# Kernel tuning notes

Measured on AMD Instinct MI355X. Metric: run time of the kernel, lower is better.

## Reference

```python
import jax, jax.numpy as jnp
import numpy as np

B, S, H = 32, 2048, 1024


def setup_inputs() -> dict:
    key = jax.random.key(0)
    ks = jax.random.split(key, 7)
    return {
        "query": jax.random.normal(ks[0], (B, 1, H), dtype=jnp.float32),
        "key": jax.random.normal(ks[1], (S, B, H), dtype=jnp.float32),
        "Wa_w": jax.random.normal(ks[2], (H, H), dtype=jnp.float32) / np.sqrt(H),
        "Wa_b": jax.random.normal(ks[3], (H,), dtype=jnp.float32) * 0.01,
        "Ua_w": jax.random.normal(ks[4], (H, H), dtype=jnp.float32) / np.sqrt(H),
        "Ua_b": jax.random.normal(ks[5], (H,), dtype=jnp.float32) * 0.01,
        "va_w": jax.random.normal(ks[6], (H,), dtype=jnp.float32) / np.sqrt(H),
        "va_b": jnp.zeros((1,), dtype=jnp.float32),
    }


def reference(query, key, Wa_w, Wa_b, Ua_w, Ua_b, va_w, va_b):
    # key: (S, B, H) -> (B, S, H)
    k = jnp.transpose(key, (1, 0, 2))
    # additive (Bahdanau) energies: tanh(Wa q + Ua k), broadcast over S
    e = jnp.tanh((query @ Wa_w + Wa_b) + (k @ Ua_w + Ua_b))  # (B, S, H)
    scores = jnp.einsum("bsh,h->bs", e, va_w) + va_b[0]       # (B, S)
    weights = jax.nn.softmax(scores, axis=-1)[:, None, :]      # (B, 1, S)
    context = jnp.einsum("bqs,bsh->bqh", weights, k)           # (B, 1, H)
    return context, weights
```

## Files before the change

### kernel.cpp

```cpp
#include <hip/hip_runtime.h>

#define Hdim 1024
#define Bdim 32
#define Sdim 2048

typedef __attribute__((ext_vector_type(8))) __bf16 bf16x8;
typedef __attribute__((ext_vector_type(4))) __bf16 bf16x4;
typedef __attribute__((ext_vector_type(4))) float f32x4;

#define GLOAD_LDS16(gp, lp)                                                              \
  __builtin_amdgcn_global_load_lds(                                                     \
      (const __attribute__((address_space(1))) unsigned int*)(gp),                      \
      (__attribute__((address_space(3))) unsigned int*)(lp), 16, 0, 0)

__global__ __launch_bounds__(256) void convert_key_kernel(const float* __restrict__ key,
                                                          __bf16* __restrict__ bkey) {
  size_t base = (size_t)blockIdx.x * 512 + threadIdx.x;
  const float4* src = (const float4*)key;
  float4 f0 = src[base];
  float4 f1 = src[base + 256];
  bf16x4 a, b;
  a[0] = (__bf16)f0.x; a[1] = (__bf16)f0.y; a[2] = (__bf16)f0.z; a[3] = (__bf16)f0.w;
  b[0] = (__bf16)f1.x; b[1] = (__bf16)f1.y; b[2] = (__bf16)f1.z; b[3] = (__bf16)f1.w;
  bf16x4* dst = (bf16x4*)bkey;
  dst[base] = a;
  dst[base + 256] = b;
}

__global__ __launch_bounds__(256) void convert_ua_kernel(const float* __restrict__ Ua,
                                                         __bf16* __restrict__ ubt) {
  int du = blockIdx.x * 256 + threadIdx.x;
  int n  = du & 127;
  int k8 = (du >> 7) & 127;
  int nt = du >> 14;
  int ng = nt * 128 + n;
  bf16x8 t;
#pragma unroll
  for (int j = 0; j < 8; ++j)
    t[j] = (__bf16)Ua[(k8 * 8 + j) * Hdim + ng];
  *(bf16x8*)(ubt + (size_t)du * 8) = t;
}

__global__ __launch_bounds__(256) void qc_kernel(const float* __restrict__ q,
                                                 const float* __restrict__ Wa,
                                                 const float* __restrict__ Wab,
                                                 const float* __restrict__ Uab,
                                                 float* __restrict__ qc) {
  int b = blockIdx.y;
  int h = blockIdx.x * 256 + threadIdx.x;
  float acc = Wab[h] + Uab[h];
  const float* qr = q + b * Hdim;
#pragma unroll 16
  for (int i = 0; i < Hdim; ++i)
    acc = fmaf(qr[i], Wa[i * Hdim + h], acc);
  qc[b * Hdim + h] = acc;
}

__global__ __launch_bounds__(256, 4) void gemm_scores_bf16_kernel(const __bf16* __restrict__ bkey,
                                                                  const __bf16* __restrict__ ubt,
                                                                  const float* __restrict__ qc,
                                                                  const float* __restrict__ va,
                                                                  float* __restrict__ part) {
  __shared__ __align__(16) __bf16 AB[2][8192];
  __shared__ float red[256];

  const int tid  = threadIdx.x;
  const int w    = tid >> 6;
  const int lane = tid & 63;
  const int quad = lane >> 4;
  const int l16  = lane & 15;

  const int l   = blockIdx.x;
  const int xcd = l & 7;
  const int i2  = l >> 3;
  const int mt  = xcd * 64 + (i2 >> 3);
  const int nt  = i2 & 7;

  const int r0 = mt * 128;
  const int n0 = nt * 128;
  const int wm = (w & 1) * 64;
  const int wn = (w >> 1) * 64;

  const __bf16* aSrc = bkey + (size_t)(r0 + (tid & 127)) * Hdim + (tid >> 7) * 8;
  const __bf16* bSrc = ubt + ((size_t)nt * 16384 + tid) * 8;

  f32x4 acc[4][4] = {};

  GLOAD_LDS16(aSrc,        &AB[0][tid * 8]);
  GLOAD_LDS16(aSrc + 16,   &AB[0][(tid + 256) * 8]);
  GLOAD_LDS16(bSrc,        &AB[0][4096 + tid * 8]);
  GLOAD_LDS16(bSrc + 2048, &AB[0][4096 + (tid + 256) * 8]);
  aSrc += 32;
  bSrc += 4096;
  __syncthreads();

  int cur = 0;
  for (int kc = 0; kc < Hdim; kc += 32) {
    if (kc + 32 < Hdim) {
      __bf16* nb = AB[cur ^ 1];
      GLOAD_LDS16(aSrc,        nb + tid * 8);
      GLOAD_LDS16(aSrc + 16,   nb + (tid + 256) * 8);
      GLOAD_LDS16(bSrc,        nb + 4096 + tid * 8);
      GLOAD_LDS16(bSrc + 2048, nb + 4096 + (tid + 256) * 8);
      aSrc += 32;
      bSrc += 4096;
    }

    const __bf16* As = AB[cur];
    const __bf16* Bs = AB[cur] + 4096;
    bf16x8 afr[4], bfr[4];
#pragma unroll
    for (int i = 0; i < 4; ++i)
      afr[i] = *(const bf16x8*)&As[(quad * 128 + wm + i * 16 + l16) * 8];
#pragma unroll
    for (int j = 0; j < 4; ++j)
      bfr[j] = *(const bf16x8*)&Bs[(quad * 128 + wn + j * 16 + l16) * 8];

#pragma unroll
    for (int i = 0; i < 4; ++i)
#pragma unroll
      for (int j = 0; j < 4; ++j)
        acc[i][j] = __builtin_amdgcn_mfma_f32_16x16x32_bf16(afr[i], bfr[j], acc[i][j], 0, 0, 0);

    __syncthreads();
    cur ^= 1;
  }

  float* qcs = (float*)AB[0];
#pragma unroll
  for (int it = 0; it < 16; ++it) {
    int u = it * 256 + tid;
    qcs[u] = qc[(u >> 7) * Hdim + n0 + (u & 127)];
  }
  __syncthreads();

  float vav[4];
#pragma unroll
  for (int j = 0; j < 4; ++j) vav[j] = va[n0 + wn + j * 16 + l16];

#pragma unroll
  for (int i = 0; i < 4; ++i) {
#pragma unroll
    for (int rg = 0; rg < 4; ++rg) {
      int b = (i & 1) * 16 + quad * 4 + rg;
      float sum = 0.f;
#pragma unroll
      for (int j = 0; j < 4; ++j) {
        float v = acc[i][j][rg] + qcs[b * 128 + wn + j * 16 + l16];
        v = fminf(fmaxf(v, -15.f), 15.f);
        float e = __expf(2.f * v);
        sum += (e - 1.f) * __builtin_amdgcn_rcpf(e + 1.f) * vav[j];
      }
#pragma unroll
      for (int off = 1; off < 16; off <<= 1)
        sum += __shfl_xor(sum, off, 64);
      if (l16 == 0)
        red[(wm + i * 16 + quad * 4 + rg) * 2 + (w >> 1)] = sum;
    }
  }
  __syncthreads();
  if (tid < 128) {
    int row = r0 + tid;
    int bb = row & 31, ss = row >> 5;
    part[((size_t)bb * Sdim + ss) * 8 + nt] = red[tid * 2] + red[tid * 2 + 1];
  }
}

__global__ __launch_bounds__(256) void gemm_scores_kernel(const float* __restrict__ key,
                                                          const __bf16* __restrict__ ubt,
                                                          const float* __restrict__ qc,
                                                          const float* __restrict__ va,
                                                          float* __restrict__ part) {
  __shared__ __align__(16) float AsQ[4096];
  __shared__ __align__(16) __bf16 Bs[4096];
  __shared__ float red[256];

  const int tid  = threadIdx.x;
  const int w    = tid >> 6;
  const int lane = tid & 63;
  const int quad = lane >> 4;
  const int l16  = lane & 15;
  const int l   = blockIdx.x;
  const int xcd = l & 7;
  const int i2  = l >> 3;
  const int mt  = xcd * 64 + (i2 >> 3);
  const int nt  = i2 & 7;
  const int r0 = mt * 128;
  const int n0 = nt * 128;
  const int wm = (w & 1) * 64;
  const int wn = (w >> 1) * 64;

  f32x4 acc[4][4] = {};

  for (int kc = 0; kc < Hdim; kc += 32) {
#pragma unroll
    for (int it = 0; it < 4; ++it) {
      int u  = it * 256 + tid;
      int k4 = u >> 7, row = u & 127;
      GLOAD_LDS16(key + (size_t)(r0 + row) * Hdim + kc + k4 * 4, AsQ + u * 4);
    }
#pragma unroll
    for (int it = 0; it < 2; ++it) {
      int u = it * 256 + tid;
      GLOAD_LDS16(ubt + ((size_t)nt * 16384 + (kc >> 3) * 128 + u) * 8, Bs + u * 8);
    }
    __syncthreads();

    bf16x8 bfr[4];
#pragma unroll
    for (int j = 0; j < 4; ++j)
      bfr[j] = *(const bf16x8*)&Bs[(quad * 128 + wn + j * 16 + l16) * 8];

    bf16x8 afr[4];
#pragma unroll
    for (int i = 0; i < 4; ++i) {
      int ml = wm + i * 16 + l16;
      float4 f0 = *(const float4*)&AsQ[((quad * 2) * 128 + ml) * 4];
      float4 f1 = *(const float4*)&AsQ[((quad * 2 + 1) * 128 + ml) * 4];
      bf16x8 a;
      a[0] = (__bf16)f0.x; a[1] = (__bf16)f0.y; a[2] = (__bf16)f0.z; a[3] = (__bf16)f0.w;
      a[4] = (__bf16)f1.x; a[5] = (__bf16)f1.y; a[6] = (__bf16)f1.z; a[7] = (__bf16)f1.w;
      afr[i] = a;
    }

#pragma unroll
    for (int i = 0; i < 4; ++i)
#pragma unroll
      for (int j = 0; j < 4; ++j)
        acc[i][j] = __builtin_amdgcn_mfma_f32_16x16x32_bf16(afr[i], bfr[j], acc[i][j], 0, 0, 0);

    __syncthreads();
  }

#pragma unroll
  for (int it = 0; it < 16; ++it) {
    int u = it * 256 + tid;
    AsQ[u] = qc[(u >> 7) * Hdim + n0 + (u & 127)];
  }
  __syncthreads();

  float vav[4];
#pragma unroll
  for (int j = 0; j < 4; ++j) vav[j] = va[n0 + wn + j * 16 + l16];

#pragma unroll
  for (int i = 0; i < 4; ++i) {
#pragma unroll
    for (int rg = 0; rg < 4; ++rg) {
      int b = (i & 1) * 16 + quad * 4 + rg;
      float sum = 0.f;
#pragma unroll
      for (int j = 0; j < 4; ++j) {
        float v = acc[i][j][rg] + AsQ[b * 128 + wn + j * 16 + l16];
        v = fminf(fmaxf(v, -15.f), 15.f);
        float e = __expf(2.f * v);
        sum += (e - 1.f) * __builtin_amdgcn_rcpf(e + 1.f) * vav[j];
      }
#pragma unroll
      for (int off = 1; off < 16; off <<= 1)
        sum += __shfl_xor(sum, off, 64);
      if (l16 == 0)
        red[(wm + i * 16 + quad * 4 + rg) * 2 + (w >> 1)] = sum;
    }
  }
  __syncthreads();
  if (tid < 128) {
    int row = r0 + tid;
    int bb = row & 31, ss = row >> 5;
    part[((size_t)bb * Sdim + ss) * 8 + nt] = red[tid * 2] + red[tid * 2 + 1];
  }
}

__global__ __launch_bounds__(256) void softmax_kernel(const float* __restrict__ part,
                                                      float* __restrict__ dout) {
  int b = blockIdx.x, t = threadIdx.x;
  int w = t >> 6, lane = t & 63;
  __shared__ float red1[4], red2[4];
  float sc[8];
  float m = -1e30f;
#pragma unroll
  for (int c = 0; c < 8; ++c) {
    int s = c * 256 + t;
    const float4* p = (const float4*)&part[((size_t)b * Sdim + s) * 8];
    float4 p0 = p[0], p1 = p[1];
    float v = ((p0.x + p0.y) + (p0.z + p0.w)) + ((p1.x + p1.y) + (p1.z + p1.w));
    sc[c] = v;
    m = fmaxf(m, v);
  }
#pragma unroll
  for (int off = 1; off < 64; off <<= 1) m = fmaxf(m, __shfl_xor(m, off, 64));
  if (lane == 0) red1[w] = m;
  __syncthreads();
  m = fmaxf(fmaxf(red1[0], red1[1]), fmaxf(red1[2], red1[3]));
  float sum = 0.f;
#pragma unroll
  for (int c = 0; c < 8; ++c) { sc[c] = __expf(sc[c] - m); sum += sc[c]; }
#pragma unroll
  for (int off = 1; off < 64; off <<= 1) sum += __shfl_xor(sum, off, 64);
  if (lane == 0) red2[w] = sum;
  __syncthreads();
  float inv = 1.f / (red2[0] + red2[1] + red2[2] + red2[3]);
#pragma unroll
  for (int c = 0; c < 8; ++c)
    dout[32768 + b * 2048 + c * 256 + t] = sc[c] * inv;
}

__global__ __launch_bounds__(256) void ctx_part_kernel(const float* __restrict__ key,
                                                       const float* __restrict__ dout,
                                                       float* __restrict__ cpart) {
  int sc = blockIdx.x;
  int b  = blockIdx.y;
  int t  = threadIdx.x;
  float4 acc = make_float4(0.f, 0.f, 0.f, 0.f);
  int s0 = sc * 64;
#pragma unroll 8
  for (int s = s0; s < s0 + 64; ++s) {
    float wgt = dout[32768 + b * 2048 + s];
    float4 k4 = *(const float4*)&key[((size_t)(s * 32 + b) << 10) + t * 4];
    acc.x = fmaf(wgt, k4.x, acc.x);
    acc.y = fmaf(wgt, k4.y, acc.y);
    acc.z = fmaf(wgt, k4.z, acc.z);
    acc.w = fmaf(wgt, k4.w, acc.w);
  }
  *(float4*)&cpart[((size_t)(sc * 32 + b) << 10) + t * 4] = acc;
}

__global__ __launch_bounds__(256) void ctx_reduce_kernel(const float* __restrict__ cpart,
                                                         float* __restrict__ dout) {
  int o = blockIdx.x * 256 + threadIdx.x;
  int b = o >> 10, h = o & 1023;
  float s = 0.f;
#pragma unroll
  for (int sc = 0; sc < 32; ++sc)
    s += cpart[((size_t)(sc * 32 + b) << 10) + h];
  dout[o] = s;
}

extern "C" void kernel_launch(void* const* d_in, const int* in_sizes, int n_in,
                              void* d_out, int out_size, void* d_ws, size_t ws_size,
                              hipStream_t stream) {
  const float* q   = (const float*)d_in[0];
  const float* key = (const float*)d_in[1];
  const float* Waw = (const float*)d_in[2];
  const float* Wab = (const float*)d_in[3];
  const float* Uaw = (const float*)d_in[4];
  const float* Uab = (const float*)d_in[5];
  const float* vaw = (const float*)d_in[6];
  float* out = (float*)d_out;

  char* ws = (char*)d_ws;
  float*  qc    = (float*)(ws);
  __bf16* ubt   = (__bf16*)(ws + 131072);
  float*  part  = (float*)(ws + 131072 + 2097152);
  float*  cpart = (float*)(ws + 131072 + 2097152 + 2097152);
  __bf16* bkey  = (__bf16*)(ws + 131072 + 2097152 + 2097152 + 4194304);
  const size_t need = 131072ull + 2097152 + 2097152 + 4194304 + 134217728;

  convert_ua_kernel<<<512, 256, 0, stream>>>(Uaw, ubt);
  qc_kernel<<<dim3(4, 32), 256, 0, stream>>>(q, Waw, Wab, Uab, qc);
  if (ws_size >= need) {
    convert_key_kernel<<<32768, 256, 0, stream>>>(key, bkey);
    gemm_scores_bf16_kernel<<<4096, 256, 0, stream>>>(bkey, ubt, qc, vaw, part);
  } else {
    gemm_scores_kernel<<<4096, 256, 0, stream>>>(key, ubt, qc, vaw, part);
  }
  softmax_kernel<<<32, 256, 0, stream>>>(part, out);
  ctx_part_kernel<<<dim3(32, 32), 256, 0, stream>>>(key, out, cpart);
  ctx_reduce_kernel<<<128, 256, 0, stream>>>(cpart, out);
}
```

Before: 681.7 us.

## Enlarge score GEMM tiles to 256x256 with phased prefetch and 8 waves

The bf16 score GEMM moves from 128x128 tiles with 4 waves to 256x256 tiles with 512 threads and K-chunks of 64. Each K-chunk is split into four phases that interleave global-to-LDS prefetch with MFMA work, using explicit vmcnt waits, raw barriers and setprio. Ua is repacked for 256-wide column tiles and the partial-score buffer shrinks from 8 to 4 column slices, which the softmax now reads. The fp32 fallback GEMM and the workspace-size check are removed, so the code now assumes the workspace is large enough. The intent is to raise operand reuse and cut global and LDS traffic per FLOP, at the cost of more LDS per block (128KB plus the reduction buffer) and lower occupancy.

Result: faster. 661.4 us (-3.0%).

```diff
diff --git a/kernel.cpp b/kernel.cpp
--- a/kernel.cpp
+++ b/kernel.cpp
@@ -12,6 +12,8 @@
   __builtin_amdgcn_global_load_lds(                                                     \
       (const __attribute__((address_space(1))) unsigned int*)(gp),                      \
       (__attribute__((address_space(3))) unsigned int*)(lp), 16, 0, 0)
+
+#define VMC(n) asm volatile("s_waitcnt vmcnt(" #n ")" ::: "memory")
 
 __global__ __launch_bounds__(256) void convert_key_kernel(const float* __restrict__ key,
                                                           __bf16* __restrict__ bkey) {
@@ -30,10 +32,10 @@
 __global__ __launch_bounds__(256) void convert_ua_kernel(const float* __restrict__ Ua,
                                                          __bf16* __restrict__ ubt) {
   int du = blockIdx.x * 256 + threadIdx.x;
-  int n  = du & 127;
-  int k8 = (du >> 7) & 127;
-  int nt = du >> 14;
-  int ng = nt * 128 + n;
+  int n  = du & 255;
+  int k8 = (du >> 8) & 127;
+  int nt = du >> 15;
+  int ng = nt * 256 + n;
   bf16x8 t;
 #pragma unroll
   for (int j = 0; j < 8; ++j)
@@ -56,13 +58,35 @@
   qc[b * Hdim + h] = acc;
 }
 
-__global__ __launch_bounds__(256, 4) void gemm_scores_bf16_kernel(const __bf16* __restrict__ bkey,
+#define PHASE(KK, MH, VMW, ...)                                                        \
+  {                                                                                    \
+    if ((MH) == 0) {                                                                   \
+      _Pragma("unroll") for (int j_ = 0; j_ < 4; ++j_)                                 \
+        bfr[j_] = *(const bf16x8*)&Bc[(((KK) * 4 + quad) * 256 + wcol + j_ * 16 + l16) * 8]; \
+    }                                                                                  \
+    _Pragma("unroll") for (int i_ = 0; i_ < 4; ++i_)                                   \
+      afr[i_] = *(const bf16x8*)&Ac[(((KK) * 4 + quad) * 256 + wrow + (MH) * 64 + i_ * 16 + l16) * 8]; \
+    __VA_ARGS__;                                                                       \
+    __builtin_amdgcn_s_barrier();                                                      \
+    asm volatile("s_waitcnt lgkmcnt(0)" ::: "memory");                                 \
+    __builtin_amdgcn_sched_barrier(0);                                                 \
+    __builtin_amdgcn_s_setprio(1);                                                     \
+    _Pragma("unroll") for (int i_ = 0; i_ < 4; ++i_)                                   \
+      _Pragma("unroll") for (int j_ = 0; j_ < 4; ++j_)                                 \
+        acc[(MH) * 4 + i_][j_] = __builtin_amdgcn_mfma_f32_16x16x32_bf16(              \
+            afr[i_], bfr[j_], acc[(MH) * 4 + i_][j_], 0, 0, 0);                        \
+    __builtin_amdgcn_s_setprio(0);                                                     \
+    VMW;                                                                               \
+    __builtin_amdgcn_s_barrier();                                                      \
+  }
+
+__global__ __launch_bounds__(512, 2) void gemm_scores_bf16_kernel(const __bf16* __restrict__ bkey,
                                                                   const __bf16* __restrict__ ubt,
                                                                   const float* __restrict__ qc,
                                                                   const float* __restrict__ va,
                                                                   float* __restrict__ part) {
-  __shared__ __align__(16) __bf16 AB[2][8192];
-  __shared__ float red[256];
+  __shared__ __align__(16) __bf16 LB[65536];
+  __shared__ __align__(16) float red[1024];
 
   const int tid  = threadIdx.x;
   const int w    = tid >> 6;
@@ -73,80 +97,90 @@
   const int l   = blockIdx.x;
   const int xcd = l & 7;
   const int i2  = l >> 3;
-  const int mt  = xcd * 64 + (i2 >> 3);
-  const int nt  = i2 & 7;
-
-  const int r0 = mt * 128;
-  const int n0 = nt * 128;
-  const int wm = (w & 1) * 64;
-  const int wn = (w >> 1) * 64;
-
-  const __bf16* aSrc = bkey + (size_t)(r0 + (tid & 127)) * Hdim + (tid >> 7) * 8;
-  const __bf16* bSrc = ubt + ((size_t)nt * 16384 + tid) * 8;
-
-  f32x4 acc[4][4] = {};
-
-  GLOAD_LDS16(aSrc,        &AB[0][tid * 8]);
-  GLOAD_LDS16(aSrc + 16,   &AB[0][(tid + 256) * 8]);
-  GLOAD_LDS16(bSrc,        &AB[0][4096 + tid * 8]);
-  GLOAD_LDS16(bSrc + 2048, &AB[0][4096 + (tid + 256) * 8]);
-  aSrc += 32;
-  bSrc += 4096;
-  __syncthreads();
+  const int mt  = xcd * 32 + (i2 >> 2);
+  const int nt  = i2 & 3;
+
+  const int r0 = mt * 256;
+  const int n0 = nt * 256;
+  const int wrow = (w & 1) * 128;
+  const int wcol = (w >> 1) * 64;
+
+  const __bf16* aS = bkey + (size_t)(r0 + (tid & 255)) * Hdim + ((tid >> 8) * 8);
+  const __bf16* bS = ubt + (size_t)nt * 262144 + (size_t)tid * 8;
+
+  f32x4 acc[8][4] = {};
+  bf16x8 afr[4], bfr[4];
+
+  GLOAD_LDS16(aS,          LB + (size_t)tid * 8);
+  GLOAD_LDS16(aS + 16,     LB + (size_t)(tid + 512) * 8);
+  GLOAD_LDS16(aS + 32,     LB + (size_t)(tid + 1024) * 8);
+  GLOAD_LDS16(aS + 48,     LB + (size_t)(tid + 1536) * 8);
+  GLOAD_LDS16(bS,          LB + 16384 + (size_t)tid * 8);
+  GLOAD_LDS16(bS + 4096,   LB + 16384 + (size_t)(tid + 512) * 8);
+  GLOAD_LDS16(bS + 8192,   LB + 16384 + (size_t)(tid + 1024) * 8);
+  GLOAD_LDS16(bS + 12288,  LB + 16384 + (size_t)(tid + 1536) * 8);
+  aS += 64;
+  bS += 16384;
+  VMC(2);
+  __builtin_amdgcn_s_barrier();
+  __builtin_amdgcn_sched_barrier(0);
 
   int cur = 0;
-  for (int kc = 0; kc < Hdim; kc += 32) {
-    if (kc + 32 < Hdim) {
-      __bf16* nb = AB[cur ^ 1];
-      GLOAD_LDS16(aSrc,        nb + tid * 8);
-      GLOAD_LDS16(aSrc + 16,   nb + (tid + 256) * 8);
-      GLOAD_LDS16(bSrc,        nb + 4096 + tid * 8);
-      GLOAD_LDS16(bSrc + 2048, nb + 4096 + (tid + 256) * 8);
-      aSrc += 32;
-      bSrc += 4096;
-    }
-
-    const __bf16* As = AB[cur];
-    const __bf16* Bs = AB[cur] + 4096;
-    bf16x8 afr[4], bfr[4];
-#pragma unroll
-    for (int i = 0; i < 4; ++i)
-      afr[i] = *(const bf16x8*)&As[(quad * 128 + wm + i * 16 + l16) * 8];
-#pragma unroll
-    for (int j = 0; j < 4; ++j)
-      bfr[j] = *(const bf16x8*)&Bs[(quad * 128 + wn + j * 16 + l16) * 8];
-
-#pragma unroll
-    for (int i = 0; i < 4; ++i)
-#pragma unroll
-      for (int j = 0; j < 4; ++j)
-        acc[i][j] = __builtin_amdgcn_mfma_f32_16x16x32_bf16(afr[i], bfr[j], acc[i][j], 0, 0, 0);
-
-    __syncthreads();
+#pragma unroll 1
+  for (int t = 0; t < 15; ++t) {
+    const __bf16* Ac = LB + cur * 32768;
+    const __bf16* Bc = Ac + 16384;
+    __bf16* An = LB + (cur ^ 1) * 32768;
+    __bf16* Bn = An + 16384;
+
+    PHASE(0, 0, (void)0,
+      GLOAD_LDS16(aS,         An + (size_t)tid * 8);
+      GLOAD_LDS16(aS + 16,    An + (size_t)(tid + 512) * 8));
+    PHASE(0, 1, VMC(4),
+      GLOAD_LDS16(aS + 32,    An + (size_t)(tid + 1024) * 8);
+      GLOAD_LDS16(aS + 48,    An + (size_t)(tid + 1536) * 8));
+    PHASE(1, 0, (void)0,
+      GLOAD_LDS16(bS,         Bn + (size_t)tid * 8);
+      GLOAD_LDS16(bS + 4096,  Bn + (size_t)(tid + 512) * 8));
+    PHASE(1, 1, VMC(2),
+      GLOAD_LDS16(bS + 8192,  Bn + (size_t)(tid + 1024) * 8);
+      GLOAD_LDS16(bS + 12288, Bn + (size_t)(tid + 1536) * 8));
+
+    aS += 64;
+    bS += 16384;
     cur ^= 1;
   }
-
-  float* qcs = (float*)AB[0];
+  {
+    const __bf16* Ac = LB + cur * 32768;
+    const __bf16* Bc = Ac + 16384;
+    PHASE(0, 0, (void)0, (void)0);
+    PHASE(0, 1, VMC(0), (void)0);
+    PHASE(1, 0, (void)0, (void)0);
+    PHASE(1, 1, (void)0, (void)0);
+  }
+
+  float* qcs = (float*)LB;
+  __syncthreads();
 #pragma unroll
   for (int it = 0; it < 16; ++it) {
-    int u = it * 256 + tid;
-    qcs[u] = qc[(u >> 7) * Hdim + n0 + (u & 127)];
+    int u = it * 512 + tid;
+    qcs[u] = qc[(u >> 8) * Hdim + n0 + (u & 255)];
   }
   __syncthreads();
 
   float vav[4];
 #pragma unroll
-  for (int j = 0; j < 4; ++j) vav[j] = va[n0 + wn + j * 16 + l16];
-
-#pragma unroll
-  for (int i = 0; i < 4; ++i) {
+  for (int j = 0; j < 4; ++j) vav[j] = va[n0 + wcol + j * 16 + l16];
+
+#pragma unroll
+  for (int mf = 0; mf < 8; ++mf) {
 #pragma unroll
     for (int rg = 0; rg < 4; ++rg) {
-      int b = (i & 1) * 16 + quad * 4 + rg;
+      int b = ((mf & 1) * 16) + quad * 4 + rg;
       float sum = 0.f;
 #pragma unroll
       for (int j = 0; j < 4; ++j) {
-        float v = acc[i][j][rg] + qcs[b * 128 + wn + j * 16 + l16];
+        float v = acc[mf][j][rg] + qcs[b * 256 + wcol + j * 16 + l16];
         v = fminf(fmaxf(v, -15.f), 15.f);
         float e = __expf(2.f * v);
         sum += (e - 1.f) * __builtin_amdgcn_rcpf(e + 1.f) * vav[j];
@@ -155,119 +189,15 @@
       for (int off = 1; off < 16; off <<= 1)
         sum += __shfl_xor(sum, off, 64);
       if (l16 == 0)
-        red[(wm + i * 16 + quad * 4 + rg) * 2 + (w >> 1)] = sum;
+        red[(wrow + mf * 16 + quad * 4 + rg) * 4 + (w >> 1)] = sum;
     }
   }
   __syncthreads();
-  if (tid < 128) {
+  if (tid < 256) {
+    const float4 r4 = *(const float4*)&red[tid * 4];
     int row = r0 + tid;
     int bb = row & 31, ss = row >> 5;
-    part[((size_t)bb * Sdim + ss) * 8 + nt] = red[tid * 2] + red[tid * 2 + 1];
-  }
-}
-
-__global__ __launch_bounds__(256) void gemm_scores_kernel(const float* __restrict__ key,
-                                                          const __bf16* __restrict__ ubt,
-                                                          const float* __restrict__ qc,
-                                                          const float* __restrict__ va,
-                                                          float* __restrict__ part) {
-  __shared__ __align__(16) float AsQ[4096];
-  __shared__ __align__(16) __bf16 Bs[4096];
-  __shared__ float red[256];
-
-  const int tid  = threadIdx.x;
-  const int w    = tid >> 6;
-  const int lane = tid & 63;
-  const int quad = lane >> 4;
-  const int l16  = lane & 15;
-  const int l   = blockIdx.x;
-  const int xcd = l & 7;
-  const int i2  = l >> 3;
-  const int mt  = xcd * 64 + (i2 >> 3);
-  const int nt  = i2 & 7;
-  const int r0 = mt * 128;
-  const int n0 = nt * 128;
-  const int wm = (w & 1) * 64;
-  const int wn = (w >> 1) * 64;
-
-  f32x4 acc[4][4] = {};
-
-  for (int kc = 0; kc < Hdim; kc += 32) {
-#pragma unroll
-    for (int it = 0; it < 4; ++it) {
-      int u  = it * 256 + tid;
-      int k4 = u >> 7, row = u & 127;
-      GLOAD_LDS16(key + (size_t)(r0 + row) * Hdim + kc + k4 * 4, AsQ + u * 4);
-    }
-#pragma unroll
-    for (int it = 0; it < 2; ++it) {
-      int u = it * 256 + tid;
-      GLOAD_LDS16(ubt + ((size_t)nt * 16384 + (kc >> 3) * 128 + u) * 8, Bs + u * 8);
-    }
-    __syncthreads();
-
-    bf16x8 bfr[4];
-#pragma unroll
-    for (int j = 0; j < 4; ++j)
-      bfr[j] = *(const bf16x8*)&Bs[(quad * 128 + wn + j * 16 + l16) * 8];
-
-    bf16x8 afr[4];
-#pragma unroll
-    for (int i = 0; i < 4; ++i) {
-      int ml = wm + i * 16 + l16;
-      float4 f0 = *(const float4*)&AsQ[((quad * 2) * 128 + ml) * 4];
-      float4 f1 = *(const float4*)&AsQ[((quad * 2 + 1) * 128 + ml) * 4];
-      bf16x8 a;
-      a[0] = (__bf16)f0.x; a[1] = (__bf16)f0.y; a[2] = (__bf16)f0.z; a[3] = (__bf16)f0.w;
-      a[4] = (__bf16)f1.x; a[5] = (__bf16)f1.y; a[6] = (__bf16)f1.z; a[7] = (__bf16)f1.w;
-      afr[i] = a;
-    }
-
-#pragma unroll
-    for (int i = 0; i < 4; ++i)
-#pragma unroll
-      for (int j = 0; j < 4; ++j)
-        acc[i][j] = __builtin_amdgcn_mfma_f32_16x16x32_bf16(afr[i], bfr[j], acc[i][j], 0, 0, 0);
-
-    __syncthreads();
-  }
-
-#pragma unroll
-  for (int it = 0; it < 16; ++it) {
-    int u = it * 256 + tid;
-    AsQ[u] = qc[(u >> 7) * Hdim + n0 + (u & 127)];
-  }
-  __syncthreads();
-
-  float vav[4];
-#pragma unroll
-  for (int j = 0; j < 4; ++j) vav[j] = va[n0 + wn + j * 16 + l16];
-
-#pragma unroll
-  for (int i = 0; i < 4; ++i) {
-#pragma unroll
-    for (int rg = 0; rg < 4; ++rg) {
-      int b = (i & 1) * 16 + quad * 4 + rg;
-      float sum = 0.f;
-#pragma unroll
-      for (int j = 0; j < 4; ++j) {
-        float v = acc[i][j][rg] + AsQ[b * 128 + wn + j * 16 + l16];
-        v = fminf(fmaxf(v, -15.f), 15.f);
-        float e = __expf(2.f * v);
-        sum += (e - 1.f) * __builtin_amdgcn_rcpf(e + 1.f) * vav[j];
-      }
-#pragma unroll
-      for (int off = 1; off < 16; off <<= 1)
-        sum += __shfl_xor(sum, off, 64);
-      if (l16 == 0)
-        red[(wm + i * 16 + quad * 4 + rg) * 2 + (w >> 1)] = sum;
-    }
-  }
-  __syncthreads();
-  if (tid < 128) {
-    int row = r0 + tid;
-    int bb = row & 31, ss = row >> 5;
-    part[((size_t)bb * Sdim + ss) * 8 + nt] = red[tid * 2] + red[tid * 2 + 1];
+    part[((size_t)bb * Sdim + ss) * 4 + nt] = (r4.x + r4.y) + (r4.z + r4.w);
   }
 }
 
@@ -281,9 +211,8 @@
 #pragma unroll
   for (int c = 0; c < 8; ++c) {
     int s = c * 256 + t;
-    const float4* p = (const float4*)&part[((size_t)b * Sdim + s) * 8];
-    float4 p0 = p[0], p1 = p[1];
-    float v = ((p0.x + p0.y) + (p0.z + p0.w)) + ((p1.x + p1.y) + (p1.z + p1.w));
+    const float4 p0 = *(const float4*)&part[((size_t)b * Sdim + s) * 4];
+    float v = (p0.x + p0.y) + (p0.z + p0.w);
     sc[c] = v;
     m = fmaxf(m, v);
   }
@@ -354,16 +283,11 @@
   float*  part  = (float*)(ws + 131072 + 2097152);
   float*  cpart = (float*)(ws + 131072 + 2097152 + 2097152);
   __bf16* bkey  = (__bf16*)(ws + 131072 + 2097152 + 2097152 + 4194304);
-  const size_t need = 131072ull + 2097152 + 2097152 + 4194304 + 134217728;
 
   convert_ua_kernel<<<512, 256, 0, stream>>>(Uaw, ubt);
   qc_kernel<<<dim3(4, 32), 256, 0, stream>>>(q, Waw, Wab, Uab, qc);
-  if (ws_size >= need) {
-    convert_key_kernel<<<32768, 256, 0, stream>>>(key, bkey);
-    gemm_scores_bf16_kernel<<<4096, 256, 0, stream>>>(bkey, ubt, qc, vaw, part);
-  } else {
-    gemm_scores_kernel<<<4096, 256, 0, stream>>>(key, ubt, qc, vaw, part);
-  }
+  convert_key_kernel<<<32768, 256, 0, stream>>>(key, bkey);
+  gemm_scores_bf16_kernel<<<1024, 512, 0, stream>>>(bkey, ubt, qc, vaw, part);
   softmax_kernel<<<32, 256, 0, stream>>>(part, out);
   ctx_part_kernel<<<dim3(32, 32), 256, 0, stream>>>(key, out, cpart);
   ctx_reduce_kernel<<<128, 256, 0, stream>>>(cpart, out);
```
